# Performance work log

Measured on AMD Instinct MI355X. Metric: run time of the kernel, lower is better.

## Reference

```python
import jax, jax.numpy as jnp
import numpy as np

NUMERICAL_STABILIZER = 1e-3


def relu_kernel(data, projection_matrix):
    # data: [B,L,H,D], projection_matrix: [M,D] -> [B,L,H,M]
    ratio = 1.0 / jnp.sqrt(jnp.asarray(projection_matrix.shape[0], dtype=data.dtype))
    data_dash = ratio * jnp.einsum('blhd,md->blhm', data, projection_matrix)
    return jax.nn.relu(data_dash) + NUMERICAL_STABILIZER


def favor_causal(query, key, value, projection_matrix):
    # query/key/value: [B,L,H,D]; projection_matrix: [M,D]
    qp = relu_kernel(query, projection_matrix)  # [B,L,H,M]
    kp = relu_kernel(key, projection_matrix)    # [B,L,H,M]
    # move L to scan axis: [L,B,H,*]
    qs = jnp.transpose(qp, (1, 0, 2, 3))
    ks = jnp.transpose(kp, (1, 0, 2, 3))
    vs = jnp.transpose(value, (1, 0, 2, 3))

    B, H, M = qs.shape[1], qs.shape[2], qs.shape[3]
    D = vs.shape[3]
    kv0 = jnp.zeros((B, H, M, D), dtype=qs.dtype)
    ksum0 = jnp.zeros((B, H, M), dtype=qs.dtype)

    def step(carry, inp):
        kv_sum, k_sum = carry
        q_t, k_t, v_t = inp  # [B,H,M], [B,H,M], [B,H,D]
        kv_sum = kv_sum + jnp.einsum('bhm,bhd->bhmd', k_t, v_t)
        k_sum = k_sum + k_t
        num_t = jnp.einsum('bhmd,bhm->bhd', kv_sum, q_t)  # [B,H,D]
        den_t = jnp.einsum('bhm,bhm->bh', q_t, k_sum)     # [B,H]
        return (kv_sum, k_sum), (num_t, den_t)

    _, (num, den) = jax.lax.scan(step, (kv0, ksum0), (qs, ks, vs))
    # num: [L,B,H,D], den: [L,B,H]
    out = num / den[..., None]
    return jnp.transpose(out, (1, 0, 2, 3))  # [B,L,H,D]


def setup_inputs() -> dict:
    key = jax.random.key(0)
    k1, k2, k3, k4 = jax.random.split(key, 4)
    B, L, H, D, M = 2, 4096, 8, 64, 128
    return {
        'query': jax.random.normal(k1, (B, L, H, D), dtype=jnp.float32),
        'key': jax.random.normal(k2, (B, L, H, D), dtype=jnp.float32),
        'value': jax.random.normal(k3, (B, L, H, D), dtype=jnp.float32),
        'projection_matrix': jax.random.normal(k4, (M, D), dtype=jnp.float32),
    }


def reference(query, key, value, projection_matrix):
    return favor_causal(query, key, value, projection_matrix)
```

## Files before the change

### kernel.cpp

```cpp
#include <hip/hip_runtime.h>


#define B_ 2
#define L_ 4096
#define H_ 8
#define D_ 64
#define M_ 128
#define BH_ 16
#define HD_ 512
#define LHD_ (L_*HD_)
#define C_ 64
#define T_ 64
#define RATIO 0.08838834764831845f
#define EPS 1e-3f

#define REC_CS 8320
#define REC_F  8192
#define CS_TOT (BH_*C_*REC_CS)
#define QF_OFF CS_TOT
#define KF_OFF (CS_TOT + BH_*C_*REC_F)

#define VT_S  72
#define KFT_S 72
#define SM_S  72

typedef __attribute__((ext_vector_type(8))) short bf16x8;
typedef __attribute__((ext_vector_type(4))) short bf16x4;
typedef __attribute__((ext_vector_type(4))) float f32x4;

__device__ __forceinline__ short f2bf(float f) {
  union { float f; unsigned u; } x; x.f = f;
  unsigned r = (x.u + 0x7fffu + ((x.u >> 16) & 1u)) >> 16;
  return (short)r;
}
__device__ __forceinline__ float bf2f(short s) {
  union { unsigned u; float f; } x; x.u = ((unsigned)(unsigned short)s) << 16;
  return x.f;
}
__device__ __forceinline__ bf16x8 load_cvt8(const float* p) {
  float4 a = *(const float4*)p;
  float4 b = *(const float4*)(p + 4);
  union { bf16x8 v; short s[8]; } u;
  u.s[0]=f2bf(a.x); u.s[1]=f2bf(a.y); u.s[2]=f2bf(a.z); u.s[3]=f2bf(a.w);
  u.s[4]=f2bf(b.x); u.s[5]=f2bf(b.y); u.s[6]=f2bf(b.z); u.s[7]=f2bf(b.w);
  return u.v;
}
#define MFMA(a,b,c) __builtin_amdgcn_mfma_f32_16x16x32_bf16((a),(b),(c),0,0,0)

__global__ __launch_bounds__(256) void p1(
    const float* __restrict__ qq, const float* __restrict__ kk,
    const float* __restrict__ vv, const float* __restrict__ P,
    unsigned short* __restrict__ ws)
{
  __shared__ short Vt[64*VT_S];
  __shared__ short Kft[128*KFT_S];

  const int tid = threadIdx.x, bid = blockIdx.x;
  const int bh = bid >> 6, c = bid & 63;
  const int b = bh >> 3, h = bh & 7;
  const int lane = tid & 63, w = tid >> 6, quad = lane >> 4, l15 = lane & 15;
  const size_t gbase = (size_t)b*LHD_ + (size_t)h*D_;
  const int t0 = c*T_;

  for (int fi = tid; fi < 64*16; fi += 256) {
    int t = fi >> 4, d4 = (fi & 15)*4;
    float4 v4 = *(const float4*)(vv + gbase + (size_t)(t0+t)*HD_ + d4);
    Vt[(d4+0)*VT_S + t] = f2bf(v4.x);
    Vt[(d4+1)*VT_S + t] = f2bf(v4.y);
    Vt[(d4+2)*VT_S + t] = f2bf(v4.z);
    Vt[(d4+3)*VT_S + t] = f2bf(v4.w);
  }

  const float* qrow = qq + gbase + (size_t)(t0 + 16*w + l15)*HD_;
  const float* krow = kk + gbase + (size_t)(t0 + 16*w + l15)*HD_;
  bf16x8 aq0 = load_cvt8(qrow + quad*8);
  bf16x8 aq1 = load_cvt8(qrow + 32 + quad*8);
  bf16x8 ak0 = load_cvt8(krow + quad*8);
  bf16x8 ak1 = load_cvt8(krow + 32 + quad*8);
  unsigned short* qfb = ws + QF_OFF + (size_t)(bh*C_+c)*REC_F;
  unsigned short* kfb = ws + KF_OFF + (size_t)(bh*C_+c)*REC_F;
  #pragma unroll
  for (int ct = 0; ct < 8; ++ct) {
    const float* prow = P + (ct*16 + l15)*64;
    bf16x8 bp0 = load_cvt8(prow + quad*8);
    bf16x8 bp1 = load_cvt8(prow + 32 + quad*8);
    f32x4 qa = {0.f,0.f,0.f,0.f}, ka = {0.f,0.f,0.f,0.f};
    qa = MFMA(aq0,bp0,qa); qa = MFMA(aq1,bp1,qa);
    ka = MFMA(ak0,bp0,ka); ka = MFMA(ak1,bp1,ka);
    #pragma unroll
    for (int reg = 0; reg < 4; ++reg) {
      int trow = 16*w + quad*4 + reg;
      int m = l15 + 16*ct;
      short qv = f2bf(fmaxf(qa[reg]*RATIO, 0.f) + EPS);
      short kv = f2bf(fmaxf(ka[reg]*RATIO, 0.f) + EPS);
      qfb[trow*128 + m] = (unsigned short)qv;
      kfb[trow*128 + m] = (unsigned short)kv;
      Kft[m*KFT_S + trow] = kv;
    }
  }
  __syncthreads();

  unsigned short* csb = ws + (size_t)(bh*C_+c)*REC_CS;
  bf16x8 av0 = *(const bf16x8*)&Vt[(16*w + l15)*VT_S + quad*8];
  bf16x8 av1 = *(const bf16x8*)&Vt[(16*w + l15)*VT_S + 32 + quad*8];
  #pragma unroll
  for (int mt = 0; mt < 8; ++mt) {
    f32x4 acc = {0.f,0.f,0.f,0.f};
    bf16x8 b0 = *(const bf16x8*)&Kft[(16*mt + l15)*KFT_S + quad*8];
    bf16x8 b1 = *(const bf16x8*)&Kft[(16*mt + l15)*KFT_S + 32 + quad*8];
    acc = MFMA(av0, b0, acc);
    acc = MFMA(av1, b1, acc);
    #pragma unroll
    for (int reg = 0; reg < 4; ++reg) {
      int d = 16*w + quad*4 + reg;
      int m = l15 + 16*mt;
      csb[d*128 + m] = (unsigned short)f2bf(acc[reg]);
    }
  }
  if (tid < 128) {
    float s = 0.f;
    #pragma unroll 8
    for (int t = 0; t < 64; ++t) s += bf2f(Kft[tid*KFT_S + t]);
    csb[64*128 + tid] = (unsigned short)f2bf(s);
  }
}

__global__ __launch_bounds__(256) void p2(unsigned short* __restrict__ ws)
{
  const int gid = blockIdx.x*256 + threadIdx.x;
  if (gid >= BH_*(REC_CS/4)) return;
  const int bh = gid / (REC_CS/4), g = gid % (REC_CS/4);
  unsigned short* base = ws + (size_t)bh*C_*REC_CS + g*4;
  float run[4] = {0.f,0.f,0.f,0.f};
  #pragma unroll 1
  for (int c = 0; c < C_; c += 4) {
    bf16x4 r[4];
    #pragma unroll
    for (int u = 0; u < 4; ++u)
      r[u] = *(const bf16x4*)(base + (size_t)(c+u)*REC_CS);
    #pragma unroll
    for (int u = 0; u < 4; ++u) {
      union { bf16x4 v; short s[4]; } wv;
      #pragma unroll
      for (int j = 0; j < 4; ++j) { wv.s[j] = f2bf(run[j]); run[j] += bf2f(r[u][j]); }
      *(bf16x4*)(base + (size_t)(c+u)*REC_CS) = wv.v;
    }
  }
}

__global__ __launch_bounds__(256) void p3(
    const float* __restrict__ vv, const unsigned short* __restrict__ ws,
    float* __restrict__ out)
{
  __shared__ short Vt[64*VT_S];
  __shared__ short Sm[64*SM_S];
  __shared__ float ks_lds[128];

  const int tid = threadIdx.x, bid = blockIdx.x;
  const int bh = bid >> 6, c = bid & 63;
  const int b = bh >> 3, h = bh & 7;
  const int lane = tid & 63, w = tid >> 6, quad = lane >> 4, l15 = lane & 15;
  const size_t gbase = (size_t)b*LHD_ + (size_t)h*D_;
  const int t0 = c*T_;
  const unsigned short* csb = ws + (size_t)(bh*C_+c)*REC_CS;
  const unsigned short* qfb = ws + QF_OFF + (size_t)(bh*C_+c)*REC_F;
  const unsigned short* kfb = ws + KF_OFF + (size_t)(bh*C_+c)*REC_F;

  for (int fi = tid; fi < 64*16; fi += 256) {
    int t = fi >> 4, d4 = (fi & 15)*4;
    float4 v4 = *(const float4*)(vv + gbase + (size_t)(t0+t)*HD_ + d4);
    Vt[(d4+0)*VT_S + t] = f2bf(v4.x);
    Vt[(d4+1)*VT_S + t] = f2bf(v4.y);
    Vt[(d4+2)*VT_S + t] = f2bf(v4.z);
    Vt[(d4+3)*VT_S + t] = f2bf(v4.w);
  }
  if (tid < 128) ks_lds[tid] = bf2f((short)csb[64*128 + tid]);

  bf16x8 qf[4];
  #pragma unroll
  for (int ks2 = 0; ks2 < 4; ++ks2)
    qf[ks2] = *(const bf16x8*)(qfb + (16*w + l15)*128 + ks2*32 + quad*8);

  __syncthreads();

  f32x4 nacc[4];
  #pragma unroll
  for (int ct = 0; ct < 4; ++ct) { f32x4 z = {0.f,0.f,0.f,0.f}; nacc[ct] = z; }
  #pragma unroll
  for (int ks2 = 0; ks2 < 4; ++ks2) {
    #pragma unroll
    for (int ct = 0; ct < 4; ++ct) {
      bf16x8 bb = *(const bf16x8*)(csb + (16*ct + l15)*128 + ks2*32 + quad*8);
      nacc[ct] = MFMA(qf[ks2], bb, nacc[ct]);
    }
  }

  float dp = 0.f;
  #pragma unroll
  for (int ks2 = 0; ks2 < 4; ++ks2)
    #pragma unroll
    for (int j = 0; j < 8; ++j)
      dp += bf2f(qf[ks2][j]) * ks_lds[ks2*32 + quad*8 + j];
  dp += __shfl_xor(dp, 16);
  dp += __shfl_xor(dp, 32);

  f32x4 sacc[4];
  #pragma unroll
  for (int jt = 0; jt < 4; ++jt) { f32x4 z = {0.f,0.f,0.f,0.f}; sacc[jt] = z; }
  #pragma unroll
  for (int ks2 = 0; ks2 < 4; ++ks2) {
    #pragma unroll
    for (int jt = 0; jt < 4; ++jt) {
      bf16x8 bb = *(const bf16x8*)(kfb + (16*jt + l15)*128 + ks2*32 + quad*8);
      sacc[jt] = MFMA(qf[ks2], bb, sacc[jt]);
    }
  }
  float rs[4] = {0.f,0.f,0.f,0.f};
  #pragma unroll
  for (int jt = 0; jt < 4; ++jt)
    #pragma unroll
    for (int reg = 0; reg < 4; ++reg) {
      int row = 16*w + quad*4 + reg;
      int j = l15 + 16*jt;
      float val = (j <= row) ? sacc[jt][reg] : 0.f;
      rs[reg] += val;
      Sm[row*SM_S + j] = f2bf(val);
    }
  #pragma unroll
  for (int reg = 0; reg < 4; ++reg) {
    rs[reg] += __shfl_xor(rs[reg], 1);
    rs[reg] += __shfl_xor(rs[reg], 2);
    rs[reg] += __shfl_xor(rs[reg], 4);
    rs[reg] += __shfl_xor(rs[reg], 8);
  }

  #pragma unroll
  for (int ks = 0; ks < 2; ++ks) {
    bf16x8 a = *(const bf16x8*)&Sm[(16*w + l15)*SM_S + ks*32 + quad*8];
    #pragma unroll
    for (int ct = 0; ct < 4; ++ct) {
      bf16x8 bb = *(const bf16x8*)&Vt[(16*ct + l15)*VT_S + ks*32 + quad*8];
      nacc[ct] = MFMA(a, bb, nacc[ct]);
    }
  }

  #pragma unroll
  for (int reg = 0; reg < 4; ++reg) {
    float den1 = __shfl(dp, 4*quad + reg);
    float inv = 1.f / (den1 + rs[reg]);
    int trow = t0 + 16*w + quad*4 + reg;
    #pragma unroll
    for (int ct = 0; ct < 4; ++ct)
      out[gbase + (size_t)trow*HD_ + 16*ct + l15] = nacc[ct][reg] * inv;
  }
}

extern "C" void kernel_launch(void* const* d_in, const int* in_sizes, int n_in,
                              void* d_out, int out_size, void* d_ws, size_t ws_size,
                              hipStream_t stream) {
  const float* q = (const float*)d_in[0];
  const float* k = (const float*)d_in[1];
  const float* v = (const float*)d_in[2];
  const float* P = (const float*)d_in[3];
  float* out = (float*)d_out;
  unsigned short* ws = (unsigned short*)d_ws;

  dim3 blk(256);
  p1<<<dim3(BH_*C_), blk, 0, stream>>>(q, k, v, P, ws);
  p2<<<dim3((BH_*(REC_CS/4) + 255)/256), blk, 0, stream>>>(ws);
  p3<<<dim3(BH_*C_), blk, 0, stream>>>(v, ws, out);
}
```

Before: 146.1 us.

## Move intra-chunk causal attention into first kernel and slim final kernel

Moves the intra-chunk QK^T masked product, row sums and S·V product from the final kernel into the first kernel, where the feature maps are already in shared memory. The partial numerators and row sums go to workspace, so the last kernel only does the inter-chunk state product and a combine. The MFMA operand order is swapped so outputs are written as vectorized bf16x4/float4 stores. The prefix-scan kernel is rewritten to one thread per element holding all 64 chunks in registers. This avoids reloading K features and V in the third kernel, at the cost of an extra fp32 numerator round trip through global memory and more LDS in the first kernel.

```diff
diff --git a/kernel.cpp b/kernel.cpp
--- a/kernel.cpp
+++ b/kernel.cpp
@@ -16,13 +16,13 @@
 
 #define REC_CS 8320
 #define REC_F  8192
-#define CS_TOT (BH_*C_*REC_CS)
-#define QF_OFF CS_TOT
-#define KF_OFF (CS_TOT + BH_*C_*REC_F)
+#define QF_OFF 8519680
+#define N2_OFF 16908288
+#define RS_OFF 25296896
 
 #define VT_S  72
 #define KFT_S 72
-#define SM_S  72
+#define TM_S  136
 
 typedef __attribute__((ext_vector_type(8))) short bf16x8;
 typedef __attribute__((ext_vector_type(4))) short bf16x4;
@@ -47,13 +47,15 @@
 }
 #define MFMA(a,b,c) __builtin_amdgcn_mfma_f32_16x16x32_bf16((a),(b),(c),0,0,0)
 
-__global__ __launch_bounds__(256) void p1(
+__global__ __launch_bounds__(256) void k1(
     const float* __restrict__ qq, const float* __restrict__ kk,
     const float* __restrict__ vv, const float* __restrict__ P,
     unsigned short* __restrict__ ws)
 {
   __shared__ short Vt[64*VT_S];
   __shared__ short Kft[128*KFT_S];
+  __shared__ short KfTM[64*TM_S];
+  __shared__ short QfTM[64*TM_S];
 
   const int tid = threadIdx.x, bid = blockIdx.x;
   const int bh = bid >> 6, c = bid & 63;
@@ -73,89 +75,155 @@
 
   const float* qrow = qq + gbase + (size_t)(t0 + 16*w + l15)*HD_;
   const float* krow = kk + gbase + (size_t)(t0 + 16*w + l15)*HD_;
-  bf16x8 aq0 = load_cvt8(qrow + quad*8);
-  bf16x8 aq1 = load_cvt8(qrow + 32 + quad*8);
-  bf16x8 ak0 = load_cvt8(krow + quad*8);
-  bf16x8 ak1 = load_cvt8(krow + 32 + quad*8);
-  unsigned short* qfb = ws + QF_OFF + (size_t)(bh*C_+c)*REC_F;
-  unsigned short* kfb = ws + KF_OFF + (size_t)(bh*C_+c)*REC_F;
+  bf16x8 bq0 = load_cvt8(qrow + quad*8);
+  bf16x8 bq1 = load_cvt8(qrow + 32 + quad*8);
+  bf16x8 bk0 = load_cvt8(krow + quad*8);
+  bf16x8 bk1 = load_cvt8(krow + 32 + quad*8);
   #pragma unroll
   for (int ct = 0; ct < 8; ++ct) {
     const float* prow = P + (ct*16 + l15)*64;
-    bf16x8 bp0 = load_cvt8(prow + quad*8);
-    bf16x8 bp1 = load_cvt8(prow + 32 + quad*8);
+    bf16x8 ap0 = load_cvt8(prow + quad*8);
+    bf16x8 ap1 = load_cvt8(prow + 32 + quad*8);
     f32x4 qa = {0.f,0.f,0.f,0.f}, ka = {0.f,0.f,0.f,0.f};
-    qa = MFMA(aq0,bp0,qa); qa = MFMA(aq1,bp1,qa);
-    ka = MFMA(ak0,bp0,ka); ka = MFMA(ak1,bp1,ka);
+    qa = MFMA(ap0,bq0,qa); qa = MFMA(ap1,bq1,qa);
+    ka = MFMA(ap0,bk0,ka); ka = MFMA(ap1,bk1,ka);
+    union { bf16x4 v; short s[4]; } pq, pk;
     #pragma unroll
     for (int reg = 0; reg < 4; ++reg) {
-      int trow = 16*w + quad*4 + reg;
-      int m = l15 + 16*ct;
+      int m = 16*ct + 4*quad + reg;
       short qv = f2bf(fmaxf(qa[reg]*RATIO, 0.f) + EPS);
       short kv = f2bf(fmaxf(ka[reg]*RATIO, 0.f) + EPS);
-      qfb[trow*128 + m] = (unsigned short)qv;
-      kfb[trow*128 + m] = (unsigned short)kv;
-      Kft[m*KFT_S + trow] = kv;
-    }
+      pq.s[reg] = qv; pk.s[reg] = kv;
+      Kft[m*KFT_S + 16*w + l15] = kv;
+    }
+    *(bf16x4*)&QfTM[(16*w+l15)*TM_S + 16*ct + 4*quad] = pq.v;
+    *(bf16x4*)&KfTM[(16*w+l15)*TM_S + 16*ct + 4*quad] = pk.v;
   }
   __syncthreads();
 
   unsigned short* csb = ws + (size_t)(bh*C_+c)*REC_CS;
-  bf16x8 av0 = *(const bf16x8*)&Vt[(16*w + l15)*VT_S + quad*8];
-  bf16x8 av1 = *(const bf16x8*)&Vt[(16*w + l15)*VT_S + 32 + quad*8];
-  #pragma unroll
-  for (int mt = 0; mt < 8; ++mt) {
-    f32x4 acc = {0.f,0.f,0.f,0.f};
-    bf16x8 b0 = *(const bf16x8*)&Kft[(16*mt + l15)*KFT_S + quad*8];
-    bf16x8 b1 = *(const bf16x8*)&Kft[(16*mt + l15)*KFT_S + 32 + quad*8];
-    acc = MFMA(av0, b0, acc);
-    acc = MFMA(av1, b1, acc);
-    #pragma unroll
-    for (int reg = 0; reg < 4; ++reg) {
-      int d = 16*w + quad*4 + reg;
-      int m = l15 + 16*mt;
-      csb[d*128 + m] = (unsigned short)f2bf(acc[reg]);
-    }
-  }
+  unsigned short* qfb = ws + QF_OFF + (size_t)(bh*C_+c)*REC_F;
+
+  {
+    int tt = tid >> 4, mb = (tid & 15)*8;
+    #pragma unroll
+    for (int j = 0; j < 4; ++j) {
+      bf16x8 v8 = *(const bf16x8*)&QfTM[(tt + 16*j)*TM_S + mb];
+      *(bf16x8*)(qfb + (tt + 16*j)*128 + mb) = v8;
+    }
+  }
+  bf16x8 qfr[4];
+  #pragma unroll
+  for (int ks2 = 0; ks2 < 4; ++ks2)
+    qfr[ks2] = *(const bf16x8*)&QfTM[(16*w+l15)*TM_S + ks2*32 + quad*8];
+
   if (tid < 128) {
     float s = 0.f;
-    #pragma unroll 8
-    for (int t = 0; t < 64; ++t) s += bf2f(Kft[tid*KFT_S + t]);
+    #pragma unroll
+    for (int i = 0; i < 8; ++i) {
+      bf16x8 r = *(const bf16x8*)&Kft[tid*KFT_S + 8*i];
+      #pragma unroll
+      for (int j = 0; j < 8; ++j) s += bf2f(r[j]);
+    }
     csb[64*128 + tid] = (unsigned short)f2bf(s);
   }
-}
-
-__global__ __launch_bounds__(256) void p2(unsigned short* __restrict__ ws)
+
+  {
+    bf16x8 av0 = *(const bf16x8*)&Vt[(16*w + l15)*VT_S + quad*8];
+    bf16x8 av1 = *(const bf16x8*)&Vt[(16*w + l15)*VT_S + 32 + quad*8];
+    #pragma unroll
+    for (int mt = 0; mt < 8; ++mt) {
+      bf16x8 b0 = *(const bf16x8*)&Kft[(16*mt + l15)*KFT_S + quad*8];
+      bf16x8 b1 = *(const bf16x8*)&Kft[(16*mt + l15)*KFT_S + 32 + quad*8];
+      f32x4 acc = {0.f,0.f,0.f,0.f};
+      acc = MFMA(b0, av0, acc);
+      acc = MFMA(b1, av1, acc);
+      union { bf16x4 v; short s[4]; } pc;
+      #pragma unroll
+      for (int reg = 0; reg < 4; ++reg) pc.s[reg] = f2bf(acc[reg]);
+      *(bf16x4*)(csb + (16*w + l15)*128 + 16*mt + 4*quad) = pc.v;
+    }
+  }
+  __syncthreads();
+
+  short* Sm = QfTM;
+
+  f32x4 sacc[4];
+  #pragma unroll
+  for (int jt = 0; jt < 4; ++jt) { f32x4 z = {0.f,0.f,0.f,0.f}; sacc[jt] = z; }
+  #pragma unroll
+  for (int ks2 = 0; ks2 < 4; ++ks2) {
+    #pragma unroll
+    for (int jt = 0; jt < 4; ++jt) {
+      bf16x8 bb = *(const bf16x8*)&KfTM[(16*jt + l15)*TM_S + ks2*32 + quad*8];
+      sacc[jt] = MFMA(qfr[ks2], bb, sacc[jt]);
+    }
+  }
+  float rs[4] = {0.f,0.f,0.f,0.f};
+  #pragma unroll
+  for (int jt = 0; jt < 4; ++jt)
+    #pragma unroll
+    for (int reg = 0; reg < 4; ++reg) {
+      int row = 16*w + 4*quad + reg;
+      int j = l15 + 16*jt;
+      float val = (j <= row) ? sacc[jt][reg] : 0.f;
+      rs[reg] += val;
+      Sm[row*TM_S + j] = f2bf(val);
+    }
+  #pragma unroll
+  for (int reg = 0; reg < 4; ++reg) {
+    rs[reg] += __shfl_xor(rs[reg], 1);
+    rs[reg] += __shfl_xor(rs[reg], 2);
+    rs[reg] += __shfl_xor(rs[reg], 4);
+    rs[reg] += __shfl_xor(rs[reg], 8);
+  }
+  float* rsg = (float*)(ws + RS_OFF);
+  if (l15 < 4) {
+    float v = (l15==0) ? rs[0] : (l15==1) ? rs[1] : (l15==2) ? rs[2] : rs[3];
+    rsg[bh*L_ + t0 + 16*w + 4*quad + l15] = v;
+  }
+
+  float* n2 = (float*)(ws + N2_OFF);
+  f32x4 nacc[4];
+  #pragma unroll
+  for (int ct = 0; ct < 4; ++ct) { f32x4 z = {0.f,0.f,0.f,0.f}; nacc[ct] = z; }
+  #pragma unroll
+  for (int kss = 0; kss < 2; ++kss) {
+    bf16x8 sb = *(const bf16x8*)&Sm[(16*w + l15)*TM_S + kss*32 + quad*8];
+    #pragma unroll
+    for (int ct = 0; ct < 4; ++ct) {
+      bf16x8 a = *(const bf16x8*)&Vt[(16*ct + l15)*VT_S + kss*32 + quad*8];
+      nacc[ct] = MFMA(a, sb, nacc[ct]);
+    }
+  }
+  const int tg = t0 + 16*w + l15;
+  #pragma unroll
+  for (int ct = 0; ct < 4; ++ct) {
+    float4 o;
+    o.x = nacc[ct][0]; o.y = nacc[ct][1]; o.z = nacc[ct][2]; o.w = nacc[ct][3];
+    *(float4*)(n2 + gbase + (size_t)tg*HD_ + 16*ct + 4*quad) = o;
+  }
+}
+
+__global__ __launch_bounds__(256) void k2(unsigned short* __restrict__ ws)
 {
   const int gid = blockIdx.x*256 + threadIdx.x;
-  if (gid >= BH_*(REC_CS/4)) return;
-  const int bh = gid / (REC_CS/4), g = gid % (REC_CS/4);
-  unsigned short* base = ws + (size_t)bh*C_*REC_CS + g*4;
-  float run[4] = {0.f,0.f,0.f,0.f};
-  #pragma unroll 1
-  for (int c = 0; c < C_; c += 4) {
-    bf16x4 r[4];
-    #pragma unroll
-    for (int u = 0; u < 4; ++u)
-      r[u] = *(const bf16x4*)(base + (size_t)(c+u)*REC_CS);
-    #pragma unroll
-    for (int u = 0; u < 4; ++u) {
-      union { bf16x4 v; short s[4]; } wv;
-      #pragma unroll
-      for (int j = 0; j < 4; ++j) { wv.s[j] = f2bf(run[j]); run[j] += bf2f(r[u][j]); }
-      *(bf16x4*)(base + (size_t)(c+u)*REC_CS) = wv.v;
-    }
-  }
-}
-
-__global__ __launch_bounds__(256) void p3(
-    const float* __restrict__ vv, const unsigned short* __restrict__ ws,
-    float* __restrict__ out)
+  const int bh = gid / REC_CS, e = gid % REC_CS;
+  unsigned short* base = ws + (size_t)bh*C_*REC_CS + e;
+  short v[64];
+  #pragma unroll
+  for (int c2 = 0; c2 < 64; ++c2) v[c2] = (short)base[(size_t)c2*REC_CS];
+  float run = 0.f;
+  #pragma unroll
+  for (int c2 = 0; c2 < 64; ++c2) {
+    base[(size_t)c2*REC_CS] = (unsigned short)f2bf(run);
+    run += bf2f(v[c2]);
+  }
+}
+
+__global__ __launch_bounds__(256) void k3(
+    const unsigned short* __restrict__ ws, float* __restrict__ out)
 {
-  __shared__ short Vt[64*VT_S];
-  __shared__ short Sm[64*SM_S];
-  __shared__ float ks_lds[128];
-
   const int tid = threadIdx.x, bid = blockIdx.x;
   const int bh = bid >> 6, c = bid & 63;
   const int b = bh >> 3, h = bh & 7;
@@ -164,94 +232,47 @@
   const int t0 = c*T_;
   const unsigned short* csb = ws + (size_t)(bh*C_+c)*REC_CS;
   const unsigned short* qfb = ws + QF_OFF + (size_t)(bh*C_+c)*REC_F;
-  const unsigned short* kfb = ws + KF_OFF + (size_t)(bh*C_+c)*REC_F;
-
-  for (int fi = tid; fi < 64*16; fi += 256) {
-    int t = fi >> 4, d4 = (fi & 15)*4;
-    float4 v4 = *(const float4*)(vv + gbase + (size_t)(t0+t)*HD_ + d4);
-    Vt[(d4+0)*VT_S + t] = f2bf(v4.x);
-    Vt[(d4+1)*VT_S + t] = f2bf(v4.y);
-    Vt[(d4+2)*VT_S + t] = f2bf(v4.z);
-    Vt[(d4+3)*VT_S + t] = f2bf(v4.w);
-  }
-  if (tid < 128) ks_lds[tid] = bf2f((short)csb[64*128 + tid]);
-
-  bf16x8 qf[4];
+  const float* n2 = (const float*)(ws + N2_OFF);
+  const float* rsg = (const float*)(ws + RS_OFF);
+
+  bf16x8 qfB[4], ksf[4];
+  #pragma unroll
+  for (int ks2 = 0; ks2 < 4; ++ks2) {
+    qfB[ks2] = *(const bf16x8*)(qfb + (16*w + l15)*128 + ks2*32 + quad*8);
+    ksf[ks2] = *(const bf16x8*)(csb + 64*128 + ks2*32 + quad*8);
+  }
+  float dp = 0.f;
   #pragma unroll
   for (int ks2 = 0; ks2 < 4; ++ks2)
-    qf[ks2] = *(const bf16x8*)(qfb + (16*w + l15)*128 + ks2*32 + quad*8);
-
-  __syncthreads();
-
-  f32x4 nacc[4];
-  #pragma unroll
-  for (int ct = 0; ct < 4; ++ct) { f32x4 z = {0.f,0.f,0.f,0.f}; nacc[ct] = z; }
-  #pragma unroll
-  for (int ks2 = 0; ks2 < 4; ++ks2) {
-    #pragma unroll
-    for (int ct = 0; ct < 4; ++ct) {
-      bf16x8 bb = *(const bf16x8*)(csb + (16*ct + l15)*128 + ks2*32 + quad*8);
-      nacc[ct] = MFMA(qf[ks2], bb, nacc[ct]);
-    }
-  }
-
-  float dp = 0.f;
-  #pragma unroll
-  for (int ks2 = 0; ks2 < 4; ++ks2)
-    #pragma unroll
-    for (int j = 0; j < 8; ++j)
-      dp += bf2f(qf[ks2][j]) * ks_lds[ks2*32 + quad*8 + j];
+    #pragma unroll
+    for (int j = 0; j < 8; ++j) dp += bf2f(qfB[ks2][j]) * bf2f(ksf[ks2][j]);
   dp += __shfl_xor(dp, 16);
   dp += __shfl_xor(dp, 32);
 
-  f32x4 sacc[4];
-  #pragma unroll
-  for (int jt = 0; jt < 4; ++jt) { f32x4 z = {0.f,0.f,0.f,0.f}; sacc[jt] = z; }
+  const int tg = t0 + 16*w + l15;
+  float rsv = rsg[bh*L_ + tg];
+  float inv = 1.f / (dp + rsv);
+
+  f32x4 nacc[4];
+  #pragma unroll
+  for (int ct = 0; ct < 4; ++ct) { f32x4 z = {0.f,0.f,0.f,0.f}; nacc[ct] = z; }
   #pragma unroll
   for (int ks2 = 0; ks2 < 4; ++ks2) {
     #pragma unroll
-    for (int jt = 0; jt < 4; ++jt) {
-      bf16x8 bb = *(const bf16x8*)(kfb + (16*jt + l15)*128 + ks2*32 + quad*8);
-      sacc[jt] = MFMA(qf[ks2], bb, sacc[jt]);
-    }
-  }
-  float rs[4] = {0.f,0.f,0.f,0.f};
-  #pragma unroll
-  for (int jt = 0; jt < 4; ++jt)
-    #pragma unroll
-    for (int reg = 0; reg < 4; ++reg) {
-      int row = 16*w + quad*4 + reg;
-      int j = l15 + 16*jt;
-      float val = (j <= row) ? sacc[jt][reg] : 0.f;
-      rs[reg] += val;
-      Sm[row*SM_S + j] = f2bf(val);
-    }
-  #pragma unroll
-  for (int reg = 0; reg < 4; ++reg) {
-    rs[reg] += __shfl_xor(rs[reg], 1);
-    rs[reg] += __shfl_xor(rs[reg], 2);
-    rs[reg] += __shfl_xor(rs[reg], 4);
-    rs[reg] += __shfl_xor(rs[reg], 8);
-  }
-
-  #pragma unroll
-  for (int ks = 0; ks < 2; ++ks) {
-    bf16x8 a = *(const bf16x8*)&Sm[(16*w + l15)*SM_S + ks*32 + quad*8];
-    #pragma unroll
     for (int ct = 0; ct < 4; ++ct) {
-      bf16x8 bb = *(const bf16x8*)&Vt[(16*ct + l15)*VT_S + ks*32 + quad*8];
-      nacc[ct] = MFMA(a, bb, nacc[ct]);
-    }
-  }
-
-  #pragma unroll
-  for (int reg = 0; reg < 4; ++reg) {
-    float den1 = __shfl(dp, 4*quad + reg);
-    float inv = 1.f / (den1 + rs[reg]);
-    int trow = t0 + 16*w + quad*4 + reg;
-    #pragma unroll
-    for (int ct = 0; ct < 4; ++ct)
-      out[gbase + (size_t)trow*HD_ + 16*ct + l15] = nacc[ct][reg] * inv;
+      bf16x8 a = *(const bf16x8*)(csb + (16*ct + l15)*128 + ks2*32 + quad*8);
+      nacc[ct] = MFMA(a, qfB[ks2], nacc[ct]);
+    }
+  }
+  #pragma unroll
+  for (int ct = 0; ct < 4; ++ct) {
+    float4 nv = *(const float4*)(n2 + gbase + (size_t)tg*HD_ + 16*ct + 4*quad);
+    float4 o;
+    o.x = (nacc[ct][0] + nv.x) * inv;
+    o.y = (nacc[ct][1] + nv.y) * inv;
+    o.z = (nacc[ct][2] + nv.z) * inv;
+    o.w = (nacc[ct][3] + nv.w) * inv;
+    *(float4*)(out + gbase + (size_t)tg*HD_ + 16*ct + 4*quad) = o;
   }
 }
 
@@ -266,7 +287,7 @@
   unsigned short* ws = (unsigned short*)d_ws;
 
   dim3 blk(256);
-  p1<<<dim3(BH_*C_), blk, 0, stream>>>(q, k, v, P, ws);
-  p2<<<dim3((BH_*(REC_CS/4) + 255)/256), blk, 0, stream>>>(ws);
-  p3<<<dim3(BH_*C_), blk, 0, stream>>>(v, ws, out);
-}
+  k1<<<dim3(BH_*C_), blk, 0, stream>>>(q, k, v, P, ws);
+  k2<<<dim3(520), blk, 0, stream>>>(ws);
+  k3<<<dim3(BH_*C_), blk, 0, stream>>>(ws, out);
+}
```

After: 139.5 us. 1.05x faster.
